# Kernel optimization log

Hardware: AMD Instinct MI355X
Metric: run time of the kernel (lower is better)

## Reference

```python
import jax, jax.numpy as jnp
import numpy as np

NEG_SLOPE = 0.01  # torch F.leaky_relu default
EPS = 1e-5        # torch BatchNorm default
N_HEADS = 8


def _bn(x, g, b):
    # BatchNorm3d in training mode: batch statistics over (N, D, H, W)
    mu = jnp.mean(x, axis=(0, 2, 3, 4), keepdims=True)
    var = jnp.var(x, axis=(0, 2, 3, 4), keepdims=True)
    xn = (x - mu) * jax.lax.rsqrt(var + EPS)
    return xn * g[None, :, None, None, None] + b[None, :, None, None, None]


def _leaky(x):
    return jnp.where(x >= 0, x, NEG_SLOPE * x)


def setup_inputs() -> dict:
    key = jax.random.key(0)
    ks = jax.random.split(key, 6)
    B, C, T, X, Y = 4, 64, 8, 96, 96
    s = 0.02
    return {
        "h": jax.random.normal(ks[0], (B, C, T, X, Y), jnp.float32),
        "conv0_w": jax.random.normal(ks[1], (C, C, 1, 3, 3), jnp.float32) * s,
        "conv0_b": jnp.zeros((C,), jnp.float32),
        "bn0_g": jnp.ones((C,), jnp.float32),
        "bn0_b": jnp.zeros((C,), jnp.float32),
        "bn1_g": jnp.ones((C,), jnp.float32),
        "bn1_b": jnp.zeros((C,), jnp.float32),
        "in_proj_w": jax.random.normal(ks[2], (3 * C, C), jnp.float32) * s,
        "in_proj_b": jnp.zeros((3 * C,), jnp.float32),
        "out_proj_w": jax.random.normal(ks[3], (C, C), jnp.float32) * s,
        "out_proj_b": jnp.zeros((C,), jnp.float32),
        "conv1_w": jax.random.normal(ks[4], (25, C), jnp.float32) * s,  # Conv1d k=1, squeezed
        "conv1_b": jnp.zeros((25,), jnp.float32),
    }


def reference(h, conv0_w, conv0_b, bn0_g, bn0_b, bn1_g, bn1_b,
              in_proj_w, in_proj_b, out_proj_w, out_proj_b, conv1_w, conv1_b):
    B, C, T, X, Y = h.shape
    H = N_HEADS
    Dh = C // H
    h_in = h

    # conv0: Conv3d kernel [1,3,3], padding [0,1,1]
    x = jax.lax.conv_general_dilated(
        h, conv0_w, window_strides=(1, 1, 1),
        padding=[(0, 0), (1, 1), (1, 1)],
        dimension_numbers=("NCDHW", "OIDHW", "NCDHW"))
    x = x + conv0_b[None, :, None, None, None]
    x = _leaky(_bn(x, bn0_g, bn0_b))

    # self-attention over the T axis; batch = B*X*Y, embed = C (torch to_mha layout)
    seq = jnp.transpose(x, (2, 0, 3, 4, 1)).reshape(T, B * X * Y, C)  # [T, N, C]
    qkv = seq @ in_proj_w.T + in_proj_b
    q, k, v = jnp.split(qkv, 3, axis=-1)
    scale = 1.0 / np.sqrt(Dh)
    q = q.reshape(T, -1, H, Dh) * jnp.asarray(scale, q.dtype)
    k = k.reshape(T, -1, H, Dh)
    v = v.reshape(T, -1, H, Dh)
    attn = jax.nn.softmax(jnp.einsum("qnhd,knhd->nhqk", q, k), axis=-1)
    o = jnp.einsum("nhqk,knhd->qnhd", attn, v).reshape(T, -1, C)
    o = o @ out_proj_w.T + out_proj_b
    # from_mha: [T, B, X, Y, C] -> [B, C, T, X, Y]
    o = jnp.transpose(o.reshape(T, B, X, Y, C), (1, 4, 0, 2, 3))

    x = _leaky(_bn(x + o, bn1_g, bn1_b))

    # spatial mean + 1x1 Conv1d -> per-(b,t) 5x5 kernels
    m = jnp.mean(x, axis=(3, 4))                                   # [B, C, T]
    kern = jnp.einsum("bct,oc->bot", m, conv1_w) + conv1_b[None, :, None]  # [B, 25, T]
    w = jnp.transpose(kern, (0, 2, 1)).reshape(B * T, 1, 5, 5)

    # dynamic depthwise conv: each (b,t) kernel applied across all C slices of h_in
    lhs = jnp.transpose(h_in, (1, 0, 2, 3, 4)).reshape(C, B * T, X, Y)  # N=C, channels=B*T
    out = jax.lax.conv_general_dilated(
        lhs, w, window_strides=(1, 1), padding=[(2, 2), (2, 2)],
        dimension_numbers=("NCHW", "OIHW", "NCHW"),
        feature_group_count=B * T)
    out = jnp.transpose(out.reshape(C, B, T, X, Y), (1, 0, 2, 3, 4))
    return out
```

## Files before the change

### kernel.cpp

```cpp
#include <hip/hip_runtime.h>
#include <hip/hip_bf16.h>

typedef __attribute__((ext_vector_type(8))) short  short8;
typedef __attribute__((ext_vector_type(4))) short  short4v;
typedef __attribute__((ext_vector_type(4))) float  floatx4;
typedef unsigned short ushort_t;
typedef __attribute__((ext_vector_type(4))) unsigned short ushort4v;
typedef __attribute__((ext_vector_type(8))) unsigned short ushort8v;
typedef __attribute__((ext_vector_type(8))) _Float16 half8;
typedef __attribute__((ext_vector_type(2))) __fp16   fp16x2;

constexpr int B_=4, C_=64, T_=8, X_=96, Y_=96;
constexpr int XY_  = X_*Y_;
constexpr int TOT_ = B_*C_*T_*XY_;
constexpr float EPS_   = 1e-5f;
constexpr float SLOPE_ = 0.01f;
constexpr float QSC_   = 0.35355339059327373f;
constexpr float INV_BN_ = 1.0f/294912.0f;
constexpr float INV_XY_ = 1.0f/9216.0f;

constexpr int HT_XSTR_  = 98*64;
constexpr int HT_BTSTR_ = 98*HT_XSTR_;
constexpr size_t HT_BYTES_ = (size_t)32*HT_BTSTR_*2;

constexpr size_t OFF_HT   = 0;
constexpr size_t OFF_X0   = HT_BYTES_ + 4096;
constexpr size_t OFF_X2   = OFF_X0 + (size_t)TOT_*2;
constexpr size_t OFF_WB   = OFF_X2 + (size_t)TOT_*2;
constexpr size_t OFF_QP   = OFF_WB + 73728;
constexpr size_t OFF_WP   = OFF_QP + 24576;
constexpr size_t OFF_SUM0 = OFF_WP + 8192;
constexpr size_t OFF_SQ0  = OFF_SUM0 + 256;
constexpr size_t OFF_SUM1 = OFF_SQ0 + 256;
constexpr size_t OFF_SQ1  = OFF_SUM1 + 256;
constexpr size_t OFF_M    = OFF_SQ1 + 256;
constexpr size_t ZBYTES   = 1024 + 8192;
constexpr size_t OFF_SC0  = OFF_M + 8192;
constexpr size_t OFF_SH0  = OFF_SC0 + 256;
constexpr size_t OFF_SC1  = OFF_SH0 + 256;
constexpr size_t OFF_SH1  = OFF_SC1 + 256;
constexpr size_t OFF_KERN = OFF_SH1 + 256;

__device__ __forceinline__ float leaky_(float v){ return v >= 0.f ? v : SLOPE_*v; }
__device__ __forceinline__ float bf2f(ushort_t u){
    union { unsigned int i; float f; } c; c.i = ((unsigned int)u) << 16; return c.f;
}
__device__ __forceinline__ ushort_t f2bf(float f){
    __hip_bfloat16 b = __float2bfloat16(f);
    return *reinterpret_cast<ushort_t*>(&b);
}
__device__ __forceinline__ ushort_t f2h(float f){
    union { __fp16 h; ushort_t u; } cv; cv.h = (__fp16)f; return cv.u;
}
__device__ __forceinline__ float h2f(ushort_t u){
    union { __fp16 h; ushort_t u; } cv; cv.u = u; return (float)cv.h;
}
__device__ __forceinline__ void gld16(const void* gp, void* lp){
    __builtin_amdgcn_global_load_lds(
        (const __attribute__((address_space(1))) void*)gp,
        (__attribute__((address_space(3))) void*)lp, 16, 0, 0);
}
union H8 { half8 h8; fp16x2 h2[4]; short8 s8; };

__global__ void k_prep(const float* __restrict__ w0, const float* __restrict__ wqkv,
                       const float* __restrict__ wo,
                       ushort_t* __restrict__ wB, short* __restrict__ qP, short* __restrict__ wP){
    int i = blockIdx.x*256 + threadIdx.x;
    if (i < 36864){
        int j = i & 7, lane = (i>>3) & 63, frag = i >> 9;
        int nt = frag & 3, kb = (frag>>2) & 1, tap = frag >> 3;
        int co = nt*16 + (lane & 15);
        int ci = kb*32 + (lane>>4)*8 + j;
        wB[i] = f2bf(w0[co*576 + ci*9 + tap]);
    } else if (i < 49152){
        int pos = i - 36864;
        int j = pos & 7, lane = (pos>>3)&63, kb = (pos>>9)&1, nt = pos>>10;
        int n = nt*16 + (lane&15);
        int c = kb*32 + (lane>>4)*8 + j;
        qP[pos] = (short)f2h(wqkv[n*64 + c]);
    } else if (i < 53248){
        int pos = i - 49152;
        int j = pos & 7, lane = (pos>>3)&63, kb = (pos>>9)&1, nt = pos>>10;
        int n = nt*16 + (lane&15);
        int c = kb*32 + (lane>>4)*8 + j;
        wP[pos] = (short)f2h(wo[n*64 + c]);
    }
}

__global__ __launch_bounds__(256) void k_hT(const float* __restrict__ h,
                                            ushort_t* __restrict__ hT){
    __shared__ float s[96*65];
    int xp = blockIdx.x, bt = blockIdx.y;
    int b = bt >> 3, t = bt & 7;
    ushort_t* opb = hT + (size_t)(bt*98 + xp)*HT_XSTR_;
    if (xp == 0 || xp == 97){
        ushort8v z8 = {0,0,0,0,0,0,0,0};
        for (int i = threadIdx.x; i < 784; i += 256)
            *(ushort8v*)(opb + i*8) = z8;
        return;
    }
    int x = xp - 1;
    int c = threadIdx.x >> 2, yq = threadIdx.x & 3;
    const float* hp = h + ((size_t)(b*64 + c)*8 + t)*9216 + x*96 + yq*24;
    #pragma unroll
    for (int i=0;i<6;i++){
        float4 v = *(const float4*)(hp + i*4);
        int y = yq*24 + i*4;
        s[(y+0)*65 + c] = v.x;
        s[(y+1)*65 + c] = v.y;
        s[(y+2)*65 + c] = v.z;
        s[(y+3)*65 + c] = v.w;
    }
    __syncthreads();
    if (threadIdx.x < 16){
        ushort8v z8 = {0,0,0,0,0,0,0,0};
        int r = (threadIdx.x < 8) ? 0 : 97;
        int o = (threadIdx.x & 7)*8;
        *(ushort8v*)(opb + r*64 + o) = z8;
    }
    ushort_t* op = opb + 64;
    int o0 = threadIdx.x*24;
    #pragma unroll
    for (int v8=0; v8<3; ++v8){
        ushort8v pk;
        #pragma unroll
        for (int j=0;j<8;j++){
            int o = o0 + v8*8 + j;
            pk[j] = f2bf(s[(o>>6)*65 + (o&63)]);
        }
        *(ushort8v*)(op + o0 + v8*8) = pk;
    }
}

__global__ __launch_bounds__(256, 2) void k_conv0(const ushort_t* __restrict__ hT,
        const ushort_t* __restrict__ wB, const float* __restrict__ bias,
        ushort_t* __restrict__ x0, float* __restrict__ sum0, float* __restrict__ sq0){
    __shared__ __align__(16) char lds[77824];
    __shared__ float red[512];
    int tid = threadIdx.x;
    int lane = tid & 63, w = tid >> 6;
    int m = lane & 15, q = lane >> 4;
    int bt = blockIdx.y, b = bt >> 3, t = bt & 7;
    int bx = blockIdx.x;
    int xr = bx*4 + w;

    {
        const char* gsrc = (const char*)(hT + ((size_t)bt*98 + bx*4)*HT_XSTR_);
        #pragma unroll
        for (int it=0; it<19; ++it){
            int lin = (tid + it*256)*16;
            int src = lin ^ (((lin>>7)&7)<<4);
            gld16(gsrc + src, lds + lin);
        }
    }
    floatx4 acc[6][4];
    #pragma unroll
    for (int nt=0; nt<4; ++nt){
        float bv = bias[nt*16 + m];
        #pragma unroll
        for (int mt=0; mt<6; ++mt) acc[mt][nt] = {bv,bv,bv,bv};
    }
    __syncthreads();

    #pragma unroll
    for (int tap=0; tap<9; ++tap){
        const int dx = tap/3, dy = tap%3;
        int rowg = (w + dx)*98 + m + dy;
        int swz  = (rowg & 7) << 4;
        #pragma unroll
        for (int kb=0; kb<2; ++kb){
            short8 bf[4];
            #pragma unroll
            for (int nt=0; nt<4; ++nt)
                bf[nt] = *(const short8*)(wB + ((tap*2+kb)*4 + nt)*512 + lane*8);
            int va = (rowg*128 + kb*64 + q*16) ^ swz;
            #pragma unroll
            for (int mt=0; mt<6; ++mt){
                short8 a = *(const short8*)(lds + va + mt*2048);
                #pragma unroll
                for (int nt=0; nt<4; ++nt)
                    acc[mt][nt] = __builtin_amdgcn_mfma_f32_16x16x32_bf16(a, bf[nt], acc[mt][nt], 0,0,0);
            }
        }
    }
    float ls[4] = {0,0,0,0}, lq[4] = {0,0,0,0};
    size_t outb = ((size_t)(b*9216 + xr*96)*8 + t)*64;
    #pragma unroll
    for (int mt=0; mt<6; ++mt){
        #pragma unroll
        for (int nt=0; nt<4; ++nt){
            #pragma unroll
            for (int r=0; r<4; ++r){
                float v = acc[mt][nt][r];
                ls[nt] += v; lq[nt] += v*v;
                int y = mt*16 + q*4 + r;
                x0[outb + (size_t)y*512 + nt*16 + m] = f2bf(v);
            }
        }
    }
    #pragma unroll
    for (int nt=0; nt<4; ++nt){
        ls[nt] += __shfl_xor(ls[nt], 16); ls[nt] += __shfl_xor(ls[nt], 32);
        lq[nt] += __shfl_xor(lq[nt], 16); lq[nt] += __shfl_xor(lq[nt], 32);
    }
    if (lane < 16){
        #pragma unroll
        for (int nt=0; nt<4; ++nt){
            red[w*64 + nt*16 + lane]       = ls[nt];
            red[256 + w*64 + nt*16 + lane] = lq[nt];
        }
    }
    __syncthreads();
    if (tid < 64){
        float a  = red[tid] + red[64+tid] + red[128+tid] + red[192+tid];
        float qq = red[256+tid] + red[320+tid] + red[384+tid] + red[448+tid];
        atomicAdd(&sum0[tid], a);
        atomicAdd(&sq0[tid], qq);
    }
}

__global__ void k_fin(const float* __restrict__ sum, const float* __restrict__ sq,
                      const float* __restrict__ g, const float* __restrict__ be,
                      float* __restrict__ scale, float* __restrict__ shift, float inv_n){
    int c = threadIdx.x;
    float mu = sum[c]*inv_n;
    float var = sq[c]*inv_n - mu*mu;
    float rs = rsqrtf(var + EPS_);
    float sc = g[c]*rs;
    scale[c] = sc; shift[c] = be[c] - mu*sc;
}

__device__ __forceinline__ void attn_f16(const ushort_t* qk, const ushort_t* vt,
        ushort_t* omdst, const fp16x2* qh, int p, int hh){
    float sv[8]; float mx = -1e30f;
    #pragma unroll
    for (int kt=0; kt<8; ++kt){
        union { short8 s; fp16x2 h[4]; } kv;
        kv.s = *(const short8*)(qk + (p*8+kt)*136 + 64 + ((hh^p)<<3));
        float s = 0.f;
        #pragma unroll
        for (int m=0;m<4;++m) s = __builtin_amdgcn_fdot2(qh[m], kv.h[m], s, false);
        sv[kt] = s; mx = fmaxf(mx, s);
    }
    float ssum = 0.f;
    #pragma unroll
    for (int kt=0;kt<8;++kt){ sv[kt] = __expf(sv[kt]-mx); ssum += sv[kt]; }
    float inv = 1.f/ssum;
    fp16x2 sp[4];
    #pragma unroll
    for (int m=0;m<4;++m) sp[m] = __builtin_amdgcn_cvt_pkrtz(sv[2*m]*inv, sv[2*m+1]*inv);
    union { short8 s; fp16x2 h[4]; } om;
    #pragma unroll
    for (int j2=0;j2<4;++j2){
        union { short8 s; fp16x2 h[4]; } v0, v1;
        v0.s = *(const short8*)(vt + (hh*8 + 2*j2    )*72 + p*8);
        v1.s = *(const short8*)(vt + (hh*8 + 2*j2 + 1)*72 + p*8);
        float o0 = 0.f, o1 = 0.f;
        #pragma unroll
        for (int m=0;m<4;++m){
            o0 = __builtin_amdgcn_fdot2(sp[m], v0.h[m], o0, false);
            o1 = __builtin_amdgcn_fdot2(sp[m], v1.h[m], o1, false);
        }
        om.h[j2] = __builtin_amdgcn_cvt_pkrtz(o0, o1);
    }
    *(short8*)omdst = om.s;
}

__global__ __launch_bounds__(256, 3) void k_attn(const ushort_t* __restrict__ x0,
        const float* __restrict__ sc0, const float* __restrict__ sh0,
        const short* __restrict__ qP, const float* __restrict__ bqkv,
        const short* __restrict__ wP, const float* __restrict__ bo,
        ushort_t* __restrict__ x2, float* __restrict__ sum1, float* __restrict__ sq1){
    __shared__ __align__(16) ushort_t smem[26624];
    ushort_t* qkA = smem;
    ushort_t* vtA = smem + 8704;
    ushort_t* qkB = smem + 13312;
    ushort_t* vtB = smem + 22016;

    int tid = threadIdx.x;
    int b = blockIdx.z, xx = blockIdx.y, y0 = blockIdx.x*16;
    size_t slabA = ((size_t)(b*9216 + xx*96 + y0)) * 512;
    size_t slabB = slabA + 4096;

    int lane = tid & 63, w = tid >> 6;
    int c16 = lane & 15, qd = lane >> 4;

    {
        int tokA = w*16 + c16;
        const ushort_t* xrA = x0 + slabA + (size_t)tokA*64;
        const ushort_t* xrB = x0 + slabB + (size_t)tokA*64;
        ushort8v xaA = *(const ushort8v*)(xrA + qd*8);
        ushort8v xbA = *(const ushort8v*)(xrA + 32 + qd*8);
        ushort8v xaB = *(const ushort8v*)(xrB + qd*8);
        ushort8v xbB = *(const ushort8v*)(xrB + 32 + qd*8);
        float sca[8], sha[8], scb[8], shb[8];
        #pragma unroll
        for (int j=0;j<8;++j){
            sca[j] = sc0[qd*8 + j];      sha[j] = sh0[qd*8 + j];
            scb[j] = sc0[32 + qd*8 + j]; shb[j] = sh0[32 + qd*8 + j];
        }
        float vA0[8], vA1[8], vB0[8], vB1[8];
        #pragma unroll
        for (int j=0;j<8;++j){
            vA0[j] = leaky_(bf2f(xaA[j])*sca[j] + sha[j]);
            vA1[j] = leaky_(bf2f(xbA[j])*scb[j] + shb[j]);
            vB0[j] = leaky_(bf2f(xaB[j])*sca[j] + sha[j]);
            vB1[j] = leaky_(bf2f(xbB[j])*scb[j] + shb[j]);
        }
        H8 a0A, a1A, a0B, a1B;
        #pragma unroll
        for (int m=0;m<4;++m){
            a0A.h2[m] = __builtin_amdgcn_cvt_pkrtz(vA0[2*m], vA0[2*m+1]);
            a1A.h2[m] = __builtin_amdgcn_cvt_pkrtz(vA1[2*m], vA1[2*m+1]);
            a0B.h2[m] = __builtin_amdgcn_cvt_pkrtz(vB0[2*m], vB0[2*m+1]);
            a1B.h2[m] = __builtin_amdgcn_cvt_pkrtz(vB1[2*m], vB1[2*m+1]);
        }
        #pragma unroll
        for (int nt=0; nt<12; ++nt){
            float bv = bqkv[nt*16 + c16];
            H8 b0, b1;
            b0.s8 = *(const short8*)(qP + (nt*2+0)*512 + lane*8);
            b1.s8 = *(const short8*)(qP + (nt*2+1)*512 + lane*8);
            floatx4 accA = {bv,bv,bv,bv};
            floatx4 accB = {bv,bv,bv,bv};
            accA = __builtin_amdgcn_mfma_f32_16x16x32_f16(a0A.h8, b0.h8, accA, 0, 0, 0);
            accB = __builtin_amdgcn_mfma_f32_16x16x32_f16(a0B.h8, b0.h8, accB, 0, 0, 0);
            accA = __builtin_amdgcn_mfma_f32_16x16x32_f16(a1A.h8, b1.h8, accA, 0, 0, 0);
            accB = __builtin_amdgcn_mfma_f32_16x16x32_f16(a1B.h8, b1.h8, accB, 0, 0, 0);
            if (nt < 4){
                #pragma unroll
                for (int r=0;r<4;++r){ accA[r]*=QSC_; accB[r]*=QSC_; }
            }
            if (nt < 8){
                int cch = nt*2 + (c16>>3);
                int sub = c16 & 7;
                #pragma unroll
                for (int r=0;r<4;++r){
                    int row = w*16 + qd*4 + r;
                    int pp = row >> 3;
                    qkA[row*136 + ((cch^pp)<<3) + sub] = f2h(accA[r]);
                    qkB[row*136 + ((cch^pp)<<3) + sub] = f2h(accB[r]);
                }
            } else {
                int chv = (nt-8)*16 + c16;
                union { fp16x2 h[2]; unsigned long long u; } pA, pB;
                pA.h[0] = __builtin_amdgcn_cvt_pkrtz(accA[0], accA[1]);
                pA.h[1] = __builtin_amdgcn_cvt_pkrtz(accA[2], accA[3]);
                pB.h[0] = __builtin_amdgcn_cvt_pkrtz(accB[0], accB[1]);
                pB.h[1] = __builtin_amdgcn_cvt_pkrtz(accB[2], accB[3]);
                *(unsigned long long*)(vtA + chv*72 + (w*16 + qd*4)) = pA.u;
                *(unsigned long long*)(vtB + chv*72 + (w*16 + qd*4)) = pB.u;
            }
        }
    }
    __syncthreads();

    {
        int tok = lane, p = tok >> 3;
        H8 qA0, qA1, qB0, qB1;
        qA0.s8 = *(const short8*)(qkA + tok*136 + ((w^p)<<3));
        qA1.s8 = *(const short8*)(qkA + tok*136 + (((w+4)^p)<<3));
        qB0.s8 = *(const short8*)(qkB + tok*136 + ((w^p)<<3));
        qB1.s8 = *(const short8*)(qkB + tok*136 + (((w+4)^p)<<3));
        attn_f16(qkA, vtA, qkA + tok*136 + ((w^p)<<3),     qA0.h2, p, w);
        attn_f16(qkB, vtB, qkB + tok*136 + ((w^p)<<3),     qB0.h2, p, w);
        attn_f16(qkA, vtA, qkA + tok*136 + (((w+4)^p)<<3), qA1.h2, p, w+4);
        attn_f16(qkB, vtB, qkB + tok*136 + (((w+4)^p)<<3), qB1.h2, p, w+4);
    }
    __syncthreads();

    {
        int row3 = w*16 + c16, p3 = row3 >> 3;
        H8 A0A, A1A, A0B, A1B;
        A0A.s8 = *(const short8*)(qkA + row3*136 + ((qd^p3)<<3));
        A1A.s8 = *(const short8*)(qkA + row3*136 + (((qd+4)^p3)<<3));
        A0B.s8 = *(const short8*)(qkB + row3*136 + ((qd^p3)<<3));
        A1B.s8 = *(const short8*)(qkB + row3*136 + (((qd+4)^p3)<<3));
        #pragma unroll
        for (int nt=0; nt<4; ++nt){
            float bv = bo[nt*16 + c16];
            H8 b0, b1;
            b0.s8 = *(const short8*)(wP + (nt*2+0)*512 + lane*8);
            b1.s8 = *(const short8*)(wP + (nt*2+1)*512 + lane*8);
            floatx4 accA = {bv,bv,bv,bv};
            floatx4 accB = {bv,bv,bv,bv};
            accA = __builtin_amdgcn_mfma_f32_16x16x32_f16(A0A.h8, b0.h8, accA, 0, 0, 0);
            accB = __builtin_amdgcn_mfma_f32_16x16x32_f16(A0B.h8, b0.h8, accB, 0, 0, 0);
            accA = __builtin_amdgcn_mfma_f32_16x16x32_f16(A1A.h8, b1.h8, accA, 0, 0, 0);
            accB = __builtin_amdgcn_mfma_f32_16x16x32_f16(A1B.h8, b1.h8, accB, 0, 0, 0);
            #pragma unroll
            for (int r=0;r<4;++r){
                int row = w*16 + qd*4 + r;
                qkA[row*136 + 64 + nt*16 + c16] = f2h(accA[r]);
                qkB[row*136 + 64 + nt*16 + c16] = f2h(accB[r]);
            }
        }
    }
    __syncthreads();

    float ls[4] = {0,0,0,0}, lq[4] = {0,0,0,0};
    #pragma unroll
    for (int it=0; it<4; ++it){
        int g = tid + it*256;
        int e0 = g*4, tk = g>>4, c0 = e0 & 63;
        floatx4 sc = *(const floatx4*)(sc0 + c0);
        floatx4 sh = *(const floatx4*)(sh0 + c0);
        ushort4v xvA = *(const ushort4v*)(x0 + slabA + e0);
        ushort4v xvB = *(const ushort4v*)(x0 + slabB + e0);
        ushort4v ovA = *(const ushort4v*)(qkA + tk*136 + 64 + c0);
        ushort4v ovB = *(const ushort4v*)(qkB + tk*136 + 64 + c0);
        ushort4v stA, stB;
        #pragma unroll
        for (int j=0;j<4;++j){
            float x1A = leaky_(bf2f(xvA[j])*sc[j] + sh[j]);
            float x1B = leaky_(bf2f(xvB[j])*sc[j] + sh[j]);
            stA[j] = f2bf(x1A + h2f(ovA[j]));
            stB[j] = f2bf(x1B + h2f(ovB[j]));
            float vA = bf2f(stA[j]), vB = bf2f(stB[j]);
            ls[j] += vA + vB; lq[j] += vA*vA + vB*vB;
        }
        *(ushort4v*)(x2 + slabA + e0) = stA;
        *(ushort4v*)(x2 + slabB + e0) = stB;
    }
    __syncthreads();
    float* red = (float*)smem;
    int slot = tid >> 4, c0s = (tid*4) & 63;
    #pragma unroll
    for (int j=0;j<4;++j){
        red[slot*64 + c0s + j]        = ls[j];
        red[1024 + slot*64 + c0s + j] = lq[j];
    }
    __syncthreads();
    if (tid < 128){
        int c = tid & 63;
        const float* base = red + (tid>>6)*1024 + c;
        float a = 0.f;
        #pragma unroll
        for (int s=0;s<16;++s) a += base[s*64];
        atomicAdd((tid < 64) ? &sum1[c] : &sq1[c], a);
    }
}

__global__ __launch_bounds__(256) void k_m(const ushort_t* __restrict__ x2,
        const float* __restrict__ sc1, const float* __restrict__ sh1,
        float* __restrict__ msum){
    __shared__ float sred[2048];
    int c = threadIdx.x & 63, tg = threadIdx.x >> 6;
    int b = blockIdx.y, chunk = blockIdx.x;
    float macc[8] = {0,0,0,0,0,0,0,0};
    float sc = sc1[c], sh = sh1[c];
    int xy_end = chunk*96 + 96;
    for (int xy = chunk*96 + tg; xy < xy_end; xy += 4){
        size_t base = ((size_t)(b*9216 + xy)*8)*64 + c;
        #pragma unroll
        for (int t=0;t<8;t++){
            float v = bf2f(x2[base + (size_t)t*64]);
            macc[t] += leaky_(v*sc + sh);
        }
    }
    #pragma unroll
    for (int t=0;t<8;t++) sred[tg*512 + t*64 + c] = macc[t];
    __syncthreads();
    #pragma unroll
    for (int i=0;i<2;++i){
        int idx = threadIdx.x + i*256;
        float a = sred[idx] + sred[512+idx] + sred[1024+idx] + sred[1536+idx];
        atomicAdd(&msum[b*512 + idx], a);
    }
}

__global__ void k_kern(const float* __restrict__ msum, const float* __restrict__ w1,
                       const float* __restrict__ b1, float* __restrict__ kern){
    int tid = blockIdx.x*256 + threadIdx.x;
    if (tid >= 800) return;
    int o = tid % 25; int t = (tid/25) % 8; int b = tid/200;
    float s = b1[o];
    const float* mrow = msum + (b*8+t)*64;
    for (int c=0;c<64;c++) s += (mrow[c]*INV_XY_) * w1[o*64+c];
    kern[(b*8+t)*25 + o] = s;
}

__global__ __launch_bounds__(256) void k_final(const float* __restrict__ h,
        const float* __restrict__ kern, float* __restrict__ out){
    __shared__ float s[100*104];
    int bct = blockIdx.x;
    int b = bct >> 9, t = bct & 7;
    int tid = threadIdx.x;
    const float* hp = h + (size_t)bct*9216;
    for (int i = tid; i < 1184; i += 256){
        int row, col;
        if (i < 416){ int r4 = i/104; row = (r4<2) ? r4 : 96 + r4; col = i - r4*104; }
        else { int j = i - 416; row = 2 + (j>>3); int k = j & 7; col = (k<4) ? k : 96 + k; }
        s[row*104 + col] = 0.f;
    }
    for (int i = tid; i < 2304; i += 256){
        int e = i*4; int xx = e/96, yy = e%96;
        float4 v = *(const float4*)(hp + e);
        *(float4*)(&s[(xx+2)*104 + yy + 4]) = v;
    }
    const float* kp = kern + ((size_t)(b*8+t))*25;
    float kv[25];
    #pragma unroll
    for (int i=0;i<25;i++) kv[i] = kp[i];
    __syncthreads();
    int tx = tid & 15, ty = tid >> 4;
    int x0 = ty*6, y0 = tx*6;
    float acc[6][6];
    #pragma unroll
    for (int i=0;i<6;i++)
        #pragma unroll
        for (int j=0;j<6;j++) acc[i][j] = 0.f;
    #pragma unroll
    for (int r=0; r<10; ++r){
        float row[10];
        const float* sp = &s[(x0+r)*104 + y0 + 2];
        #pragma unroll
        for (int c=0;c<10;c++) row[c] = sp[c];
        #pragma unroll
        for (int orow=0; orow<6; ++orow){
            if (orow > r || orow < r-4) continue;
            int dx = r - orow;
            #pragma unroll
            for (int dy=0; dy<5; ++dy){
                float wv = kv[dx*5+dy];
                #pragma unroll
                for (int oc=0; oc<6; ++oc)
                    acc[orow][oc] += wv * row[oc+dy];
            }
        }
    }
    float* op = out + (size_t)bct*9216 + x0*96 + y0;
    #pragma unroll
    for (int orow=0; orow<6; ++orow)
        #pragma unroll
        for (int oc=0; oc<6; ++oc)
            op[orow*96 + oc] = acc[orow][oc];
}

extern "C" void kernel_launch(void* const* d_in, const int* in_sizes, int n_in,
                              void* d_out, int out_size, void* d_ws, size_t ws_size,
                              hipStream_t stream){
    const float* h    = (const float*)d_in[0];
    const float* w0   = (const float*)d_in[1];
    const float* cb0  = (const float*)d_in[2];
    const float* bn0g = (const float*)d_in[3];
    const float* bn0b = (const float*)d_in[4];
    const float* bn1g = (const float*)d_in[5];
    const float* bn1b = (const float*)d_in[6];
    const float* wqkv = (const float*)d_in[7];
    const float* bqkv = (const float*)d_in[8];
    const float* wo   = (const float*)d_in[9];
    const float* bo   = (const float*)d_in[10];
    const float* w1   = (const float*)d_in[11];
    const float* b1   = (const float*)d_in[12];

    char* ws = (char*)d_ws;
    ushort_t* hT  = (ushort_t*)(ws + OFF_HT);
    ushort_t* x0  = (ushort_t*)(ws + OFF_X0);
    ushort_t* x2  = (ushort_t*)(ws + OFF_X2);
    ushort_t* wB  = (ushort_t*)(ws + OFF_WB);
    short* qP     = (short*)(ws + OFF_QP);
    short* wP     = (short*)(ws + OFF_WP);
    float* sum0   = (float*)(ws + OFF_SUM0);
    float* sq0    = (float*)(ws + OFF_SQ0);
    float* sum1   = (float*)(ws + OFF_SUM1);
    float* sq1    = (float*)(ws + OFF_SQ1);
    float* msum   = (float*)(ws + OFF_M);
    float* sc0    = (float*)(ws + OFF_SC0);
    float* sh0    = (float*)(ws + OFF_SH0);
    float* sc1    = (float*)(ws + OFF_SC1);
    float* sh1    = (float*)(ws + OFF_SH1);
    float* kern   = (float*)(ws + OFF_KERN);
    float* outp   = (float*)d_out;

    (void)hipMemsetAsync(ws + OFF_SUM0, 0, ZBYTES, stream);
    k_prep  <<<208, 256, 0, stream>>>(w0, wqkv, wo, wB, qP, wP);
    k_hT    <<<dim3(98, 32), 256, 0, stream>>>(h, hT);
    k_conv0 <<<dim3(24, 32), 256, 0, stream>>>(hT, wB, cb0, x0, sum0, sq0);
    k_fin   <<<1, 64, 0, stream>>>(sum0, sq0, bn0g, bn0b, sc0, sh0, INV_BN_);
    k_attn  <<<dim3(6, 96, 4), 256, 0, stream>>>(x0, sc0, sh0, qP, bqkv, wP, bo, x2, sum1, sq1);
    k_fin   <<<1, 64, 0, stream>>>(sum1, sq1, bn1g, bn1b, sc1, sh1, INV_BN_);
    k_m     <<<dim3(96, 4), 256, 0, stream>>>(x2, sc1, sh1, msum);
    k_kern  <<<4, 256, 0, stream>>>(msum, w1, b1, kern);
    k_final <<<2048, 256, 0, stream>>>(h, kern, outp);
}
```

Measured before the change: 322.5 us.

## Make attention blocks persistent over three slabs with prefetch; vectorize k_m loads

Each attention block now handles three 16-token slab pairs in a loop instead of one. It prefetches the next slab's input and the residual x0 values into registers while the current slab's attention runs, and it accumulates the BN statistics across iterations, so there is one atomic reduction per block. The grid shrinks from 2304 to 768 blocks, which amortizes setup and atomics but lowers parallelism and raises register pressure. Separately, k_m now reads 8 channels per thread with vector loads instead of scalar strided loads.

```diff
diff --git a/kernel.cpp b/kernel.cpp
--- a/kernel.cpp
+++ b/kernel.cpp
@@ -278,151 +278,172 @@
     ushort_t* vtB = smem + 22016;
 
     int tid = threadIdx.x;
-    int b = blockIdx.z, xx = blockIdx.y, y0 = blockIdx.x*16;
-    size_t slabA = ((size_t)(b*9216 + xx*96 + y0)) * 512;
-    size_t slabB = slabA + 4096;
+    int b = blockIdx.z, xx = blockIdx.y, y0 = blockIdx.x*48;
+    size_t base = ((size_t)(b*9216 + xx*96 + y0)) * 512;
 
     int lane = tid & 63, w = tid >> 6;
     int c16 = lane & 15, qd = lane >> 4;
-
-    {
-        int tokA = w*16 + c16;
-        const ushort_t* xrA = x0 + slabA + (size_t)tokA*64;
-        const ushort_t* xrB = x0 + slabB + (size_t)tokA*64;
-        ushort8v xaA = *(const ushort8v*)(xrA + qd*8);
-        ushort8v xbA = *(const ushort8v*)(xrA + 32 + qd*8);
-        ushort8v xaB = *(const ushort8v*)(xrB + qd*8);
-        ushort8v xbB = *(const ushort8v*)(xrB + 32 + qd*8);
-        float sca[8], sha[8], scb[8], shb[8];
-        #pragma unroll
-        for (int j=0;j<8;++j){
-            sca[j] = sc0[qd*8 + j];      sha[j] = sh0[qd*8 + j];
-            scb[j] = sc0[32 + qd*8 + j]; shb[j] = sh0[32 + qd*8 + j];
-        }
-        float vA0[8], vA1[8], vB0[8], vB1[8];
-        #pragma unroll
-        for (int j=0;j<8;++j){
-            vA0[j] = leaky_(bf2f(xaA[j])*sca[j] + sha[j]);
-            vA1[j] = leaky_(bf2f(xbA[j])*scb[j] + shb[j]);
-            vB0[j] = leaky_(bf2f(xaB[j])*sca[j] + sha[j]);
-            vB1[j] = leaky_(bf2f(xbB[j])*scb[j] + shb[j]);
-        }
-        H8 a0A, a1A, a0B, a1B;
-        #pragma unroll
-        for (int m=0;m<4;++m){
-            a0A.h2[m] = __builtin_amdgcn_cvt_pkrtz(vA0[2*m], vA0[2*m+1]);
-            a1A.h2[m] = __builtin_amdgcn_cvt_pkrtz(vA1[2*m], vA1[2*m+1]);
-            a0B.h2[m] = __builtin_amdgcn_cvt_pkrtz(vB0[2*m], vB0[2*m+1]);
-            a1B.h2[m] = __builtin_amdgcn_cvt_pkrtz(vB1[2*m], vB1[2*m+1]);
-        }
-        #pragma unroll
-        for (int nt=0; nt<12; ++nt){
-            float bv = bqkv[nt*16 + c16];
-            H8 b0, b1;
-            b0.s8 = *(const short8*)(qP + (nt*2+0)*512 + lane*8);
-            b1.s8 = *(const short8*)(qP + (nt*2+1)*512 + lane*8);
-            floatx4 accA = {bv,bv,bv,bv};
-            floatx4 accB = {bv,bv,bv,bv};
-            accA = __builtin_amdgcn_mfma_f32_16x16x32_f16(a0A.h8, b0.h8, accA, 0, 0, 0);
-            accB = __builtin_amdgcn_mfma_f32_16x16x32_f16(a0B.h8, b0.h8, accB, 0, 0, 0);
-            accA = __builtin_amdgcn_mfma_f32_16x16x32_f16(a1A.h8, b1.h8, accA, 0, 0, 0);
-            accB = __builtin_amdgcn_mfma_f32_16x16x32_f16(a1B.h8, b1.h8, accB, 0, 0, 0);
-            if (nt < 4){
-                #pragma unroll
-                for (int r=0;r<4;++r){ accA[r]*=QSC_; accB[r]*=QSC_; }
-            }
-            if (nt < 8){
-                int cch = nt*2 + (c16>>3);
-                int sub = c16 & 7;
+    int tokA = w*16 + c16;
+
+    float sca[8], sha[8], scb[8], shb[8];
+    #pragma unroll
+    for (int j=0;j<8;++j){
+        sca[j] = sc0[qd*8 + j];      sha[j] = sh0[qd*8 + j];
+        scb[j] = sc0[32 + qd*8 + j]; shb[j] = sh0[32 + qd*8 + j];
+    }
+    const ushort_t* xr0 = x0 + base + (size_t)tokA*64;
+    ushort8v pfA0 = *(const ushort8v*)(xr0 + qd*8);
+    ushort8v pfA1 = *(const ushort8v*)(xr0 + 32 + qd*8);
+    ushort8v pfB0 = *(const ushort8v*)(xr0 + 4096 + qd*8);
+    ushort8v pfB1 = *(const ushort8v*)(xr0 + 4096 + 32 + qd*8);
+
+    float ls[4] = {0,0,0,0}, lq[4] = {0,0,0,0};
+
+    #pragma unroll 1
+    for (int iter=0; iter<3; ++iter){
+        size_t slabA = base + (size_t)iter*8192;
+        size_t slabB = slabA + 4096;
+
+        {
+            float vA0[8], vA1[8], vB0[8], vB1[8];
+            #pragma unroll
+            for (int j=0;j<8;++j){
+                vA0[j] = leaky_(bf2f(pfA0[j])*sca[j] + sha[j]);
+                vA1[j] = leaky_(bf2f(pfA1[j])*scb[j] + shb[j]);
+                vB0[j] = leaky_(bf2f(pfB0[j])*sca[j] + sha[j]);
+                vB1[j] = leaky_(bf2f(pfB1[j])*scb[j] + shb[j]);
+            }
+            H8 a0A, a1A, a0B, a1B;
+            #pragma unroll
+            for (int m=0;m<4;++m){
+                a0A.h2[m] = __builtin_amdgcn_cvt_pkrtz(vA0[2*m], vA0[2*m+1]);
+                a1A.h2[m] = __builtin_amdgcn_cvt_pkrtz(vA1[2*m], vA1[2*m+1]);
+                a0B.h2[m] = __builtin_amdgcn_cvt_pkrtz(vB0[2*m], vB0[2*m+1]);
+                a1B.h2[m] = __builtin_amdgcn_cvt_pkrtz(vB1[2*m], vB1[2*m+1]);
+            }
+            #pragma unroll
+            for (int nt=0; nt<12; ++nt){
+                float bv = bqkv[nt*16 + c16];
+                H8 b0, b1;
+                b0.s8 = *(const short8*)(qP + (nt*2+0)*512 + lane*8);
+                b1.s8 = *(const short8*)(qP + (nt*2+1)*512 + lane*8);
+                floatx4 accA = {bv,bv,bv,bv};
+                floatx4 accB = {bv,bv,bv,bv};
+                accA = __builtin_amdgcn_mfma_f32_16x16x32_f16(a0A.h8, b0.h8, accA, 0, 0, 0);
+                accB = __builtin_amdgcn_mfma_f32_16x16x32_f16(a0B.h8, b0.h8, accB, 0, 0, 0);
+                accA = __builtin_amdgcn_mfma_f32_16x16x32_f16(a1A.h8, b1.h8, accA, 0, 0, 0);
+                accB = __builtin_amdgcn_mfma_f32_16x16x32_f16(a1B.h8, b1.h8, accB, 0, 0, 0);
+                if (nt < 4){
+                    #pragma unroll
+                    for (int r=0;r<4;++r){ accA[r]*=QSC_; accB[r]*=QSC_; }
+                }
+                if (nt < 8){
+                    int cch = nt*2 + (c16>>3);
+                    int sub = c16 & 7;
+                    #pragma unroll
+                    for (int r=0;r<4;++r){
+                        int row = w*16 + qd*4 + r;
+                        int pp = row >> 3;
+                        qkA[row*136 + ((cch^pp)<<3) + sub] = f2h(accA[r]);
+                        qkB[row*136 + ((cch^pp)<<3) + sub] = f2h(accB[r]);
+                    }
+                } else {
+                    int chv = (nt-8)*16 + c16;
+                    union { fp16x2 h[2]; unsigned long long u; } pA, pB;
+                    pA.h[0] = __builtin_amdgcn_cvt_pkrtz(accA[0], accA[1]);
+                    pA.h[1] = __builtin_amdgcn_cvt_pkrtz(accA[2], accA[3]);
+                    pB.h[0] = __builtin_amdgcn_cvt_pkrtz(accB[0], accB[1]);
+                    pB.h[1] = __builtin_amdgcn_cvt_pkrtz(accB[2], accB[3]);
+                    *(unsigned long long*)(vtA + chv*72 + (w*16 + qd*4)) = pA.u;
+                    *(unsigned long long*)(vtB + chv*72 + (w*16 + qd*4)) = pB.u;
+                }
+            }
+        }
+        ushort4v p4A[4], p4B[4];
+        #pragma unroll
+        for (int it=0; it<4; ++it){
+            int e0 = (tid + it*256)*4;
+            p4A[it] = *(const ushort4v*)(x0 + slabA + e0);
+            p4B[it] = *(const ushort4v*)(x0 + slabB + e0);
+        }
+        if (iter < 2){
+            const ushort_t* xrn = x0 + base + (size_t)(iter+1)*8192 + (size_t)tokA*64;
+            pfA0 = *(const ushort8v*)(xrn + qd*8);
+            pfA1 = *(const ushort8v*)(xrn + 32 + qd*8);
+            pfB0 = *(const ushort8v*)(xrn + 4096 + qd*8);
+            pfB1 = *(const ushort8v*)(xrn + 4096 + 32 + qd*8);
+        }
+        __syncthreads();
+
+        {
+            int tok = lane, p = tok >> 3;
+            H8 qA0, qA1, qB0, qB1;
+            qA0.s8 = *(const short8*)(qkA + tok*136 + ((w^p)<<3));
+            qA1.s8 = *(const short8*)(qkA + tok*136 + (((w+4)^p)<<3));
+            qB0.s8 = *(const short8*)(qkB + tok*136 + ((w^p)<<3));
+            qB1.s8 = *(const short8*)(qkB + tok*136 + (((w+4)^p)<<3));
+            attn_f16(qkA, vtA, qkA + tok*136 + ((w^p)<<3),     qA0.h2, p, w);
+            attn_f16(qkB, vtB, qkB + tok*136 + ((w^p)<<3),     qB0.h2, p, w);
+            attn_f16(qkA, vtA, qkA + tok*136 + (((w+4)^p)<<3), qA1.h2, p, w+4);
+            attn_f16(qkB, vtB, qkB + tok*136 + (((w+4)^p)<<3), qB1.h2, p, w+4);
+        }
+        __syncthreads();
+
+        {
+            int row3 = w*16 + c16, p3 = row3 >> 3;
+            H8 A0A, A1A, A0B, A1B;
+            A0A.s8 = *(const short8*)(qkA + row3*136 + ((qd^p3)<<3));
+            A1A.s8 = *(const short8*)(qkA + row3*136 + (((qd+4)^p3)<<3));
+            A0B.s8 = *(const short8*)(qkB + row3*136 + ((qd^p3)<<3));
+            A1B.s8 = *(const short8*)(qkB + row3*136 + (((qd+4)^p3)<<3));
+            #pragma unroll
+            for (int nt=0; nt<4; ++nt){
+                float bv = bo[nt*16 + c16];
+                H8 b0, b1;
+                b0.s8 = *(const short8*)(wP + (nt*2+0)*512 + lane*8);
+                b1.s8 = *(const short8*)(wP + (nt*2+1)*512 + lane*8);
+                floatx4 accA = {bv,bv,bv,bv};
+                floatx4 accB = {bv,bv,bv,bv};
+                accA = __builtin_amdgcn_mfma_f32_16x16x32_f16(A0A.h8, b0.h8, accA, 0, 0, 0);
+                accB = __builtin_amdgcn_mfma_f32_16x16x32_f16(A0B.h8, b0.h8, accB, 0, 0, 0);
+                accA = __builtin_amdgcn_mfma_f32_16x16x32_f16(A1A.h8, b1.h8, accA, 0, 0, 0);
+                accB = __builtin_amdgcn_mfma_f32_16x16x32_f16(A1B.h8, b1.h8, accB, 0, 0, 0);
                 #pragma unroll
                 for (int r=0;r<4;++r){
                     int row = w*16 + qd*4 + r;
-                    int pp = row >> 3;
-                    qkA[row*136 + ((cch^pp)<<3) + sub] = f2h(accA[r]);
-                    qkB[row*136 + ((cch^pp)<<3) + sub] = f2h(accB[r]);
+                    qkA[row*136 + 64 + nt*16 + c16] = f2h(accA[r]);
+                    qkB[row*136 + 64 + nt*16 + c16] = f2h(accB[r]);
                 }
-            } else {
-                int chv = (nt-8)*16 + c16;
-                union { fp16x2 h[2]; unsigned long long u; } pA, pB;
-                pA.h[0] = __builtin_amdgcn_cvt_pkrtz(accA[0], accA[1]);
-                pA.h[1] = __builtin_amdgcn_cvt_pkrtz(accA[2], accA[3]);
-                pB.h[0] = __builtin_amdgcn_cvt_pkrtz(accB[0], accB[1]);
-                pB.h[1] = __builtin_amdgcn_cvt_pkrtz(accB[2], accB[3]);
-                *(unsigned long long*)(vtA + chv*72 + (w*16 + qd*4)) = pA.u;
-                *(unsigned long long*)(vtB + chv*72 + (w*16 + qd*4)) = pB.u;
-            }
-        }
-    }
-    __syncthreads();
-
-    {
-        int tok = lane, p = tok >> 3;
-        H8 qA0, qA1, qB0, qB1;
-        qA0.s8 = *(const short8*)(qkA + tok*136 + ((w^p)<<3));
-        qA1.s8 = *(const short8*)(qkA + tok*136 + (((w+4)^p)<<3));
-        qB0.s8 = *(const short8*)(qkB + tok*136 + ((w^p)<<3));
-        qB1.s8 = *(const short8*)(qkB + tok*136 + (((w+4)^p)<<3));
-        attn_f16(qkA, vtA, qkA + tok*136 + ((w^p)<<3),     qA0.h2, p, w);
-        attn_f16(qkB, vtB, qkB + tok*136 + ((w^p)<<3),     qB0.h2, p, w);
-        attn_f16(qkA, vtA, qkA + tok*136 + (((w+4)^p)<<3), qA1.h2, p, w+4);
-        attn_f16(qkB, vtB, qkB + tok*136 + (((w+4)^p)<<3), qB1.h2, p, w+4);
-    }
-    __syncthreads();
-
-    {
-        int row3 = w*16 + c16, p3 = row3 >> 3;
-        H8 A0A, A1A, A0B, A1B;
-        A0A.s8 = *(const short8*)(qkA + row3*136 + ((qd^p3)<<3));
-        A1A.s8 = *(const short8*)(qkA + row3*136 + (((qd+4)^p3)<<3));
-        A0B.s8 = *(const short8*)(qkB + row3*136 + ((qd^p3)<<3));
-        A1B.s8 = *(const short8*)(qkB + row3*136 + (((qd+4)^p3)<<3));
-        #pragma unroll
-        for (int nt=0; nt<4; ++nt){
-            float bv = bo[nt*16 + c16];
-            H8 b0, b1;
-            b0.s8 = *(const short8*)(wP + (nt*2+0)*512 + lane*8);
-            b1.s8 = *(const short8*)(wP + (nt*2+1)*512 + lane*8);
-            floatx4 accA = {bv,bv,bv,bv};
-            floatx4 accB = {bv,bv,bv,bv};
-            accA = __builtin_amdgcn_mfma_f32_16x16x32_f16(A0A.h8, b0.h8, accA, 0, 0, 0);
-            accB = __builtin_amdgcn_mfma_f32_16x16x32_f16(A0B.h8, b0.h8, accB, 0, 0, 0);
-            accA = __builtin_amdgcn_mfma_f32_16x16x32_f16(A1A.h8, b1.h8, accA, 0, 0, 0);
-            accB = __builtin_amdgcn_mfma_f32_16x16x32_f16(A1B.h8, b1.h8, accB, 0, 0, 0);
-            #pragma unroll
-            for (int r=0;r<4;++r){
-                int row = w*16 + qd*4 + r;
-                qkA[row*136 + 64 + nt*16 + c16] = f2h(accA[r]);
-                qkB[row*136 + 64 + nt*16 + c16] = f2h(accB[r]);
-            }
-        }
-    }
-    __syncthreads();
-
-    float ls[4] = {0,0,0,0}, lq[4] = {0,0,0,0};
-    #pragma unroll
-    for (int it=0; it<4; ++it){
-        int g = tid + it*256;
-        int e0 = g*4, tk = g>>4, c0 = e0 & 63;
-        floatx4 sc = *(const floatx4*)(sc0 + c0);
-        floatx4 sh = *(const floatx4*)(sh0 + c0);
-        ushort4v xvA = *(const ushort4v*)(x0 + slabA + e0);
-        ushort4v xvB = *(const ushort4v*)(x0 + slabB + e0);
-        ushort4v ovA = *(const ushort4v*)(qkA + tk*136 + 64 + c0);
-        ushort4v ovB = *(const ushort4v*)(qkB + tk*136 + 64 + c0);
-        ushort4v stA, stB;
-        #pragma unroll
-        for (int j=0;j<4;++j){
-            float x1A = leaky_(bf2f(xvA[j])*sc[j] + sh[j]);
-            float x1B = leaky_(bf2f(xvB[j])*sc[j] + sh[j]);
-            stA[j] = f2bf(x1A + h2f(ovA[j]));
-            stB[j] = f2bf(x1B + h2f(ovB[j]));
-            float vA = bf2f(stA[j]), vB = bf2f(stB[j]);
-            ls[j] += vA + vB; lq[j] += vA*vA + vB*vB;
-        }
-        *(ushort4v*)(x2 + slabA + e0) = stA;
-        *(ushort4v*)(x2 + slabB + e0) = stB;
-    }
-    __syncthreads();
+            }
+        }
+        __syncthreads();
+
+        #pragma unroll
+        for (int it=0; it<4; ++it){
+            int g = tid + it*256;
+            int e0 = g*4, tk = g>>4, c0 = e0 & 63;
+            floatx4 sc = *(const floatx4*)(sc0 + c0);
+            floatx4 sh = *(const floatx4*)(sh0 + c0);
+            ushort4v xvA = p4A[it];
+            ushort4v xvB = p4B[it];
+            ushort4v ovA = *(const ushort4v*)(qkA + tk*136 + 64 + c0);
+            ushort4v ovB = *(const ushort4v*)(qkB + tk*136 + 64 + c0);
+            ushort4v stA, stB;
+            #pragma unroll
+            for (int j=0;j<4;++j){
+                float x1A = leaky_(bf2f(xvA[j])*sc[j] + sh[j]);
+                float x1B = leaky_(bf2f(xvB[j])*sc[j] + sh[j]);
+                stA[j] = f2bf(x1A + h2f(ovA[j]));
+                stB[j] = f2bf(x1B + h2f(ovB[j]));
+                float vA = bf2f(stA[j]), vB = bf2f(stB[j]);
+                ls[j] += vA + vB; lq[j] += vA*vA + vB*vB;
+            }
+            *(ushort4v*)(x2 + slabA + e0) = stA;
+            *(ushort4v*)(x2 + slabB + e0) = stB;
+        }
+        __syncthreads();
+    }
+
     float* red = (float*)smem;
     int slot = tid >> 4, c0s = (tid*4) & 63;
     #pragma unroll
@@ -433,10 +454,10 @@
     __syncthreads();
     if (tid < 128){
         int c = tid & 63;
-        const float* base = red + (tid>>6)*1024 + c;
+        const float* base2 = red + (tid>>6)*1024 + c;
         float a = 0.f;
         #pragma unroll
-        for (int s=0;s<16;++s) a += base[s*64];
+        for (int s=0;s<16;++s) a += base2[s*64];
         atomicAdd((tid < 64) ? &sum1[c] : &sq1[c], a);
     }
 }
@@ -445,21 +466,23 @@
         const float* __restrict__ sc1, const float* __restrict__ sh1,
         float* __restrict__ msum){
     __shared__ float sred[2048];
-    int c = threadIdx.x & 63, tg = threadIdx.x >> 6;
+    int c8 = threadIdx.x & 7, t = (threadIdx.x>>3)&7, tg = threadIdx.x >> 6;
     int b = blockIdx.y, chunk = blockIdx.x;
     float macc[8] = {0,0,0,0,0,0,0,0};
-    float sc = sc1[c], sh = sh1[c];
+    float scv[8], shv[8];
+    #pragma unroll
+    for (int j=0;j<8;++j){ scv[j] = sc1[c8*8+j]; shv[j] = sh1[c8*8+j]; }
     int xy_end = chunk*96 + 96;
     for (int xy = chunk*96 + tg; xy < xy_end; xy += 4){
-        size_t base = ((size_t)(b*9216 + xy)*8)*64 + c;
-        #pragma unroll
-        for (int t=0;t<8;t++){
-            float v = bf2f(x2[base + (size_t)t*64]);
-            macc[t] += leaky_(v*sc + sh);
-        }
-    }
-    #pragma unroll
-    for (int t=0;t<8;t++) sred[tg*512 + t*64 + c] = macc[t];
+        ushort8v v8 = *(const ushort8v*)(x2 + ((size_t)(b*9216 + xy)*8 + t)*64 + c8*8);
+        #pragma unroll
+        for (int j=0;j<8;++j){
+            float v = bf2f(v8[j]);
+            macc[j] += leaky_(v*scv[j] + shv[j]);
+        }
+    }
+    #pragma unroll
+    for (int j=0;j<8;++j) sred[tg*512 + t*64 + c8*8 + j] = macc[j];
     __syncthreads();
     #pragma unroll
     for (int i=0;i<2;++i){
@@ -578,7 +601,7 @@
     k_hT    <<<dim3(98, 32), 256, 0, stream>>>(h, hT);
     k_conv0 <<<dim3(24, 32), 256, 0, stream>>>(hT, wB, cb0, x0, sum0, sq0);
     k_fin   <<<1, 64, 0, stream>>>(sum0, sq0, bn0g, bn0b, sc0, sh0, INV_BN_);
-    k_attn  <<<dim3(6, 96, 4), 256, 0, stream>>>(x0, sc0, sh0, qP, bqkv, wP, bo, x2, sum1, sq1);
+    k_attn  <<<dim3(2, 96, 4), 256, 0, stream>>>(x0, sc0, sh0, qP, bqkv, wP, bo, x2, sum1, sq1);
     k_fin   <<<1, 64, 0, stream>>>(sum1, sq1, bn1g, bn1b, sc1, sh1, INV_BN_);
     k_m     <<<dim3(96, 4), 256, 0, stream>>>(x2, sc1, sh1, msum);
     k_kern  <<<4, 256, 0, stream>>>(msum, w1, b1, kern);
```

After: 362.8 us. +12.5%, slower.
